# Optimization experiments

Hardware: AMD Instinct MI355X
Metric: run time of the kernel (lower is better)

## Reference

```python
import jax, jax.numpy as jnp
import numpy as np

N_NODES = 100000


def _gcn_norm(edge_index, num_nodes):
    # add self loops
    src, dst = edge_index[0], edge_index[1]
    loop = jnp.arange(num_nodes, dtype=src.dtype)
    row = jnp.concatenate([src, loop])  # [E+N]
    col = jnp.concatenate([dst, loop])
    ew = jnp.ones(row.shape[0], dtype=jnp.float32)
    deg = jax.ops.segment_sum(ew, col, num_segments=num_nodes)  # [N]
    dinv = jnp.where(deg > 0, jax.lax.rsqrt(deg), 0.0)
    norm = dinv[row] * ew * dinv[col]  # [E+N]
    return row, col, norm


def setup_inputs() -> dict:
    key = jax.random.key(0)
    k1, k2, k3 = jax.random.split(key, 3)
    x = jax.random.normal(k1, (N_NODES, 64), dtype=jnp.float32)
    edge_index = jax.random.randint(k2, (2, 1280000), 0, N_NODES, dtype=jnp.int64)
    W = jax.random.normal(k3, (40, 64), dtype=jnp.float32) * (1.0 / np.sqrt(64))
    b = jnp.zeros((40,), dtype=jnp.float32)
    return {"x": x, "edge_index": edge_index, "W": W, "b": b}


def reference(x, edge_index, W, b):
    K = 3
    row, col, norm = _gcn_norm(edge_index, N_NODES)
    h = x
    for _ in range(K):
        # gather from source nodes, scale by symmetric norm, scatter-add to dst
        msg = norm[:, None] * h[row]  # [E+N, F]
        h = jax.ops.segment_sum(msg, col, num_segments=N_NODES)
    logits = h @ W.T + b  # [N, C]
    return jax.nn.log_softmax(logits, axis=1)
```

## Files before the change

### kernel.cpp

```cpp
#include <hip/hip_runtime.h>

#define F_IN 64
#define F_OUT 40
#define USTRIDE 20
#define QPN 5

#define PART_BLK 256
#define PART_EPB 16
#define PART_TILE (PART_BLK * PART_EPB)
#define BSHIFT 8
#define BCAP 4096
#define MAXB 512

#define WSTRIDE 17

__device__ inline unsigned pk2(float x, float y) {
    unsigned a = __float_as_uint(x); a = (a + 0x7FFFu + ((a >> 16) & 1u)) >> 16;
    unsigned b = __float_as_uint(y); b = (b + 0x7FFFu + ((b >> 16) & 1u)) >> 16;
    return a | (b << 16);
}
__device__ inline void up2(unsigned u, float& a, float& b) {
    a = __uint_as_float(u << 16); b = __uint_as_float(u & 0xFFFF0000u);
}

__global__ void bucket_init_kernel(int* __restrict__ bfill, int nbk) {
    int b = blockIdx.x * blockDim.x + threadIdx.x;
    if (b < nbk) bfill[b] = b * BCAP;
}

__global__ __launch_bounds__(PART_BLK) void partition_kernel(const int* __restrict__ src,
                                                             const int* __restrict__ dst,
                                                             int* __restrict__ bfill,
                                                             unsigned* __restrict__ staging,
                                                             int E, int nbk) {
    __shared__ int hist[MAXB];
    __shared__ int base[MAXB];
    int tid = threadIdx.x;
    for (int b = tid; b < nbk; b += PART_BLK) hist[b] = 0;
    __syncthreads();

    int rank[PART_EPB];
    int bk[PART_EPB];
    unsigned rec[PART_EPB];
    int eb = blockIdx.x * PART_TILE + tid;
#pragma unroll
    for (int k = 0; k < PART_EPB; ++k) {
        int e = eb + k * PART_BLK;
        if (e < E) {
            int r = src[e];
            int c = dst[e];
            int b = c >> BSHIFT;
            bk[k] = b;
            rec[k] = (unsigned)r | ((unsigned)(c & 255) << 17);
            rank[k] = atomicAdd(&hist[b], 1);
        } else {
            bk[k] = -1;
        }
    }
    __syncthreads();
    for (int b = tid; b < nbk; b += PART_BLK) {
        int h = hist[b];
        base[b] = h ? atomicAdd(&bfill[b], h) : 0;
    }
    __syncthreads();
#pragma unroll
    for (int k = 0; k < PART_EPB; ++k) {
        if (bk[k] >= 0) staging[base[bk[k]] + rank[k]] = rec[k];
    }
}

__global__ __launch_bounds__(512) void btotal_scan_kernel(const int* __restrict__ bfill,
                                                          int* __restrict__ ebase,
                                                          int* __restrict__ rowptr_end,
                                                          int nbk, int E) {
    __shared__ int s[512];
    int tid = threadIdx.x;
    int v = (tid < nbk) ? (bfill[tid] - tid * BCAP) : 0;
    s[tid] = v;
    __syncthreads();
    for (int off = 1; off < 512; off <<= 1) {
        int t = (tid >= off) ? s[tid - off] : 0;
        __syncthreads();
        s[tid] += t;
        __syncthreads();
    }
    if (tid < nbk) ebase[tid] = s[tid] - v;
    if (tid == 0) *rowptr_end = E;
}

__global__ __launch_bounds__(256) void bucket_finalize_kernel(const unsigned* __restrict__ staging,
                                                              const int* __restrict__ bfill,
                                                              const int* __restrict__ ebase,
                                                              int* __restrict__ rowptr,
                                                              int* __restrict__ deg,
                                                              float* __restrict__ dinv,
                                                              float* __restrict__ dinv2,
                                                              int* __restrict__ srcs, int n) {
    int b = blockIdx.x;
    __shared__ int h[256];
    __shared__ int cur[256];
    int tid = threadIdx.x;
    h[tid] = 0;
    __syncthreads();

    int cnt = bfill[b] - b * BCAP;
    const unsigned* rec = staging + (size_t)b * BCAP;
    for (int i = tid; i < cnt; i += 256) {
        atomicAdd(&h[rec[i] >> 17], 1);
    }
    __syncthreads();

    int v = h[tid];
    for (int off = 1; off < 256; off <<= 1) {
        int t = (tid >= off) ? h[tid - off] : 0;
        __syncthreads();
        h[tid] += t;
        __syncthreads();
    }
    int excl = h[tid] - v;
    int base = ebase[b];
    int node = (b << BSHIFT) | tid;
    if (node < n) {
        rowptr[node] = base + excl;
        deg[node] = v;
        float r = rsqrtf((float)v + 1.0f);
        dinv[node] = r;
        dinv2[node] = r * r;
    }
    cur[tid] = base + excl;
    __syncthreads();

    for (int i = tid; i < cnt; i += 256) {
        unsigned rv = rec[i];
        int pos = atomicAdd(&cur[rv >> 17], 1);
        srcs[pos] = (int)(rv & 0x1FFFFu);
    }
}

__global__ __launch_bounds__(256, 6) void proj_kernel(const float* __restrict__ x,
                                                      const float* __restrict__ W,
                                                      const float* __restrict__ dinv,
                                                      unsigned* __restrict__ u, int n) {
    __shared__ float Ws[F_OUT * WSTRIDE * 4];
    for (int i = threadIdx.x; i < F_OUT * F_IN; i += 256) {
        int c = i >> 6;
        int k = i & 63;
        Ws[c * (WSTRIDE * 4) + k] = W[i];
    }
    __syncthreads();

    int t = blockIdx.x * 256 + threadIdx.x;
    int node = t >> 2;
    int q = t & 3;
    if (node >= n) return;

    const float4* xp = (const float4*)(x + (size_t)node * F_IN);
    const float4* Wq = (const float4*)Ws + (size_t)(q * 10) * WSTRIDE;

    float acc[10];
#pragma unroll
    for (int c = 0; c < 10; ++c) acc[c] = 0.0f;

#pragma unroll 1
    for (int f4 = 0; f4 < F_IN / 4; ++f4) {
        float4 xv = xp[f4];
#pragma unroll
        for (int c = 0; c < 10; ++c) {
            float4 w = Wq[c * WSTRIDE + f4];
            acc[c] += xv.x * w.x + xv.y * w.y + xv.z * w.z + xv.w * w.w;
        }
    }

    float dv = dinv[node];
    unsigned* up = u + (size_t)node * USTRIDE + q * 5;
#pragma unroll
    for (int j = 0; j < 5; ++j) {
        up[j] = pk2(dv * acc[2 * j], dv * acc[2 * j + 1]);
    }
}

__global__ __launch_bounds__(256) void propagate_kernel(const int* __restrict__ rowptr,
                                                        const int* __restrict__ srcs,
                                                        const float* __restrict__ dinv2,
                                                        const unsigned* __restrict__ ucur,
                                                        unsigned* __restrict__ unew, int n) {
    int t = blockIdx.x * blockDim.x + threadIdx.x;
    int node = t / QPN;
    int q = t - node * QPN;
    if (node >= n) return;

    int beg = rowptr[node];
    int end = rowptr[node + 1];

    const uint4* U = (const uint4*)ucur;
    uint4 sv = U[(size_t)node * QPN + q];
    float a0, a1, a2, a3, a4, a5, a6, a7;
    up2(sv.x, a0, a1); up2(sv.y, a2, a3); up2(sv.z, a4, a5); up2(sv.w, a6, a7);

    int i = beg;
    for (; i + 3 < end; i += 4) {
        int s0 = srcs[i], s1 = srcs[i + 1], s2 = srcs[i + 2], s3 = srcs[i + 3];
        uint4 v0 = U[(size_t)s0 * QPN + q];
        uint4 v1 = U[(size_t)s1 * QPN + q];
        uint4 v2 = U[(size_t)s2 * QPN + q];
        uint4 v3 = U[(size_t)s3 * QPN + q];
        float b0, b1;
        up2(v0.x, b0, b1); a0 += b0; a1 += b1;
        up2(v0.y, b0, b1); a2 += b0; a3 += b1;
        up2(v0.z, b0, b1); a4 += b0; a5 += b1;
        up2(v0.w, b0, b1); a6 += b0; a7 += b1;
        up2(v1.x, b0, b1); a0 += b0; a1 += b1;
        up2(v1.y, b0, b1); a2 += b0; a3 += b1;
        up2(v1.z, b0, b1); a4 += b0; a5 += b1;
        up2(v1.w, b0, b1); a6 += b0; a7 += b1;
        up2(v2.x, b0, b1); a0 += b0; a1 += b1;
        up2(v2.y, b0, b1); a2 += b0; a3 += b1;
        up2(v2.z, b0, b1); a4 += b0; a5 += b1;
        up2(v2.w, b0, b1); a6 += b0; a7 += b1;
        up2(v3.x, b0, b1); a0 += b0; a1 += b1;
        up2(v3.y, b0, b1); a2 += b0; a3 += b1;
        up2(v3.z, b0, b1); a4 += b0; a5 += b1;
        up2(v3.w, b0, b1); a6 += b0; a7 += b1;
    }
    for (; i < end; ++i) {
        uint4 v = U[(size_t)srcs[i] * QPN + q];
        float b0, b1;
        up2(v.x, b0, b1); a0 += b0; a1 += b1;
        up2(v.y, b0, b1); a2 += b0; a3 += b1;
        up2(v.z, b0, b1); a4 += b0; a5 += b1;
        up2(v.w, b0, b1); a6 += b0; a7 += b1;
    }

    float ds = dinv2[node];
    uint4 o;
    o.x = pk2(ds * a0, ds * a1);
    o.y = pk2(ds * a2, ds * a3);
    o.z = pk2(ds * a4, ds * a5);
    o.w = pk2(ds * a6, ds * a7);
    ((uint4*)unew)[(size_t)node * QPN + q] = o;
}

__global__ void logsoftmax_kernel(const unsigned* __restrict__ u, float* __restrict__ out,
                                  const float* __restrict__ bias,
                                  const int* __restrict__ deg, int n) {
    int node = blockIdx.x * blockDim.x + threadIdx.x;
    if (node >= n) return;
    float sq = sqrtf((float)deg[node] + 1.0f);
    const uint4* up = (const uint4*)(u + (size_t)node * USTRIDE);
    float v[F_OUT];
#pragma unroll
    for (int g = 0; g < 5; ++g) {
        uint4 t = up[g];
        float a, b2;
        up2(t.x, a, b2); v[8 * g + 0] = sq * a + bias[8 * g + 0];
                         v[8 * g + 1] = sq * b2 + bias[8 * g + 1];
        up2(t.y, a, b2); v[8 * g + 2] = sq * a + bias[8 * g + 2];
                         v[8 * g + 3] = sq * b2 + bias[8 * g + 3];
        up2(t.z, a, b2); v[8 * g + 4] = sq * a + bias[8 * g + 4];
                         v[8 * g + 5] = sq * b2 + bias[8 * g + 5];
        up2(t.w, a, b2); v[8 * g + 6] = sq * a + bias[8 * g + 6];
                         v[8 * g + 7] = sq * b2 + bias[8 * g + 7];
    }
    float mx = -1e30f;
#pragma unroll
    for (int c = 0; c < F_OUT; ++c) mx = fmaxf(mx, v[c]);
    float se = 0.0f;
#pragma unroll
    for (int c = 0; c < F_OUT; ++c) se += __expf(v[c] - mx);
    float lse = mx + __logf(se);
    float4* p = (float4*)(out + (size_t)node * F_OUT);
#pragma unroll
    for (int c4 = 0; c4 < F_OUT / 4; ++c4) {
        float4 t;
        t.x = v[4 * c4 + 0] - lse; t.y = v[4 * c4 + 1] - lse;
        t.z = v[4 * c4 + 2] - lse; t.w = v[4 * c4 + 3] - lse;
        p[c4] = t;
    }
}

extern "C" void kernel_launch(void* const* d_in, const int* in_sizes, int n_in,
                              void* d_out, int out_size, void* d_ws, size_t ws_size,
                              hipStream_t stream) {
    const float* x  = (const float*)d_in[0];
    const int*   ei = (const int*)d_in[1];
    const float* W  = (const float*)d_in[2];
    const float* b  = (const float*)d_in[3];

    const int N = in_sizes[0] / F_IN;
    const int E = in_sizes[1] / 2;
    const int* src = ei;
    const int* dst = ei + E;
    const int nbk = (N + (1 << BSHIFT) - 1) >> BSHIFT;

    char* base = (char*)d_ws;
    size_t off = 0;
    auto alloc = [&](size_t bytes) {
        char* p = base + off;
        off = (off + bytes + 255) & ~(size_t)255;
        return p;
    };
    int*      deg_i   = (int*)     alloc((size_t)N * 4);
    float*    dinv    = (float*)   alloc((size_t)N * 4);
    float*    dinv2   = (float*)   alloc((size_t)N * 4);
    int*      rowptr  = (int*)     alloc((size_t)(N + 1) * 4);
    int*      bfill   = (int*)     alloc((size_t)MAXB * 4);
    int*      ebase   = (int*)     alloc((size_t)MAXB * 4);
    unsigned* staging = (unsigned*)alloc((size_t)nbk * BCAP * 4);
    int*      srcs_s  = (int*)     alloc((size_t)E * 4);
    unsigned* uA      = (unsigned*)alloc((size_t)N * USTRIDE * 4);
    unsigned* uB      = (unsigned*)alloc((size_t)N * USTRIDE * 4);
    float*    outp    = (float*)d_out;

    bucket_init_kernel<<<(nbk + 255) / 256, 256, 0, stream>>>(bfill, nbk);
    partition_kernel<<<(E + PART_TILE - 1) / PART_TILE, PART_BLK, 0, stream>>>(
        src, dst, bfill, staging, E, nbk);

    btotal_scan_kernel<<<1, 512, 0, stream>>>(bfill, ebase, rowptr + N, nbk, E);
    bucket_finalize_kernel<<<nbk, 256, 0, stream>>>(staging, bfill, ebase, rowptr,
                                                    deg_i, dinv, dinv2, srcs_s, N);

    proj_kernel<<<((size_t)N * 4 + 255) / 256, 256, 0, stream>>>(x, W, dinv, uA, N);

    const int pt = N * QPN;
    const int pg = (pt + 255) / 256;
    propagate_kernel<<<pg, 256, 0, stream>>>(rowptr, srcs_s, dinv2, uA, uB, N);
    propagate_kernel<<<pg, 256, 0, stream>>>(rowptr, srcs_s, dinv2, uB, uA, N);
    propagate_kernel<<<pg, 256, 0, stream>>>(rowptr, srcs_s, dinv2, uA, uB, N);

    logsoftmax_kernel<<<(N + 255) / 256, 256, 0, stream>>>(uB, outp, b, deg_i, N);
}
```

Before: 218.1 us.

## Degree-sort nodes within buckets for propagation and process two nodes per thread in projection

Measured after the change: 245.1 us. 1.12x slower.

```diff
diff --git a/kernel.cpp b/kernel.cpp
--- a/kernel.cpp
+++ b/kernel.cpp
@@ -21,11 +21,6 @@
 }
 __device__ inline void up2(unsigned u, float& a, float& b) {
     a = __uint_as_float(u << 16); b = __uint_as_float(u & 0xFFFF0000u);
-}
-
-__global__ void bucket_init_kernel(int* __restrict__ bfill, int nbk) {
-    int b = blockIdx.x * blockDim.x + threadIdx.x;
-    if (b < nbk) bfill[b] = b * BCAP;
 }
 
 __global__ __launch_bounds__(PART_BLK) void partition_kernel(const int* __restrict__ src,
@@ -60,7 +55,7 @@
     __syncthreads();
     for (int b = tid; b < nbk; b += PART_BLK) {
         int h = hist[b];
-        base[b] = h ? atomicAdd(&bfill[b], h) : 0;
+        base[b] = h ? (b * BCAP + atomicAdd(&bfill[b], h)) : 0;
     }
     __syncthreads();
 #pragma unroll
@@ -75,7 +70,7 @@
                                                           int nbk, int E) {
     __shared__ int s[512];
     int tid = threadIdx.x;
-    int v = (tid < nbk) ? (bfill[tid] - tid * BCAP) : 0;
+    int v = (tid < nbk) ? bfill[tid] : 0;
     s[tid] = v;
     __syncthreads();
     for (int off = 1; off < 512; off <<= 1) {
@@ -95,15 +90,17 @@
                                                               int* __restrict__ deg,
                                                               float* __restrict__ dinv,
                                                               float* __restrict__ dinv2,
-                                                              int* __restrict__ srcs, int n) {
+                                                              int* __restrict__ srcs,
+                                                              int* __restrict__ perm, int n) {
     int b = blockIdx.x;
     __shared__ int h[256];
     __shared__ int cur[256];
+    __shared__ unsigned keys[256];
     int tid = threadIdx.x;
     h[tid] = 0;
     __syncthreads();
 
-    int cnt = bfill[b] - b * BCAP;
+    int cnt = bfill[b];
     const unsigned* rec = staging + (size_t)b * BCAP;
     for (int i = tid; i < cnt; i += 256) {
         atomicAdd(&h[rec[i] >> 17], 1);
@@ -111,6 +108,8 @@
     __syncthreads();
 
     int v = h[tid];
+    keys[tid] = ((unsigned)v << 8) | (unsigned)(255 - tid);
+
     for (int off = 1; off < 256; off <<= 1) {
         int t = (tid >= off) ? h[tid - off] : 0;
         __syncthreads();
@@ -135,9 +134,27 @@
         int pos = atomicAdd(&cur[rv >> 17], 1);
         srcs[pos] = (int)(rv & 0x1FFFFu);
     }
-}
-
-__global__ __launch_bounds__(256, 6) void proj_kernel(const float* __restrict__ x,
+    __syncthreads();
+
+    for (int k = 2; k <= 256; k <<= 1) {
+        for (int j = k >> 1; j > 0; j >>= 1) {
+            int p = tid ^ j;
+            if (p > tid) {
+                unsigned a = keys[tid];
+                unsigned c = keys[p];
+                bool asc_region = ((tid & k) == 0);
+                if (asc_region ? (a < c) : (a > c)) {
+                    keys[tid] = c;
+                    keys[p] = a;
+                }
+            }
+            __syncthreads();
+        }
+    }
+    perm[(b << BSHIFT) | tid] = (b << BSHIFT) | (int)(255u - (keys[tid] & 255u));
+}
+
+__global__ __launch_bounds__(256, 4) void proj_kernel(const float* __restrict__ x,
                                                       const float* __restrict__ W,
                                                       const float* __restrict__ dinv,
                                                       unsigned* __restrict__ u, int n) {
@@ -150,44 +167,54 @@
     __syncthreads();
 
     int t = blockIdx.x * 256 + threadIdx.x;
-    int node = t >> 2;
+    int g = t >> 2;
     int q = t & 3;
-    if (node >= n) return;
-
-    const float4* xp = (const float4*)(x + (size_t)node * F_IN);
-    const float4* Wq = (const float4*)Ws + (size_t)(q * 10) * WSTRIDE;
-
-    float acc[10];
-#pragma unroll
-    for (int c = 0; c < 10; ++c) acc[c] = 0.0f;
+    int n0 = 2 * g;
+    if (n0 >= n) return;
+    int n1 = n0 + 1;
+
+    const float4* xp0 = (const float4*)(x + (size_t)n0 * F_IN);
+    const float4* xp1 = (const float4*)(x + (size_t)n1 * F_IN);
+    const float4* Wq  = (const float4*)Ws + (size_t)(q * 10) * WSTRIDE;
+
+    float acc0[10], acc1[10];
+#pragma unroll
+    for (int c = 0; c < 10; ++c) { acc0[c] = 0.0f; acc1[c] = 0.0f; }
 
 #pragma unroll 1
     for (int f4 = 0; f4 < F_IN / 4; ++f4) {
-        float4 xv = xp[f4];
+        float4 x0 = xp0[f4];
+        float4 x1 = xp1[f4];
 #pragma unroll
         for (int c = 0; c < 10; ++c) {
             float4 w = Wq[c * WSTRIDE + f4];
-            acc[c] += xv.x * w.x + xv.y * w.y + xv.z * w.z + xv.w * w.w;
+            acc0[c] += x0.x * w.x + x0.y * w.y + x0.z * w.z + x0.w * w.w;
+            acc1[c] += x1.x * w.x + x1.y * w.y + x1.z * w.z + x1.w * w.w;
         }
     }
 
-    float dv = dinv[node];
-    unsigned* up = u + (size_t)node * USTRIDE + q * 5;
+    float d0 = dinv[n0];
+    float d1 = dinv[n1];
+    unsigned* up0 = u + (size_t)n0 * USTRIDE + q * 5;
+    unsigned* up1 = u + (size_t)n1 * USTRIDE + q * 5;
 #pragma unroll
     for (int j = 0; j < 5; ++j) {
-        up[j] = pk2(dv * acc[2 * j], dv * acc[2 * j + 1]);
-    }
-}
-
-__global__ __launch_bounds__(256) void propagate_kernel(const int* __restrict__ rowptr,
+        up0[j] = pk2(d0 * acc0[2 * j], d0 * acc0[2 * j + 1]);
+        up1[j] = pk2(d1 * acc1[2 * j], d1 * acc1[2 * j + 1]);
+    }
+}
+
+__global__ __launch_bounds__(256) void propagate_kernel(const int* __restrict__ perm,
+                                                        const int* __restrict__ rowptr,
                                                         const int* __restrict__ srcs,
                                                         const float* __restrict__ dinv2,
                                                         const unsigned* __restrict__ ucur,
                                                         unsigned* __restrict__ unew, int n) {
     int t = blockIdx.x * blockDim.x + threadIdx.x;
-    int node = t / QPN;
-    int q = t - node * QPN;
-    if (node >= n) return;
+    int g = t / QPN;
+    int q = t - g * QPN;
+    if (g >= n) return;
+    int node = perm[g];
 
     int beg = rowptr[node];
     int end = rowptr[node + 1];
@@ -305,27 +332,28 @@
     int*      rowptr  = (int*)     alloc((size_t)(N + 1) * 4);
     int*      bfill   = (int*)     alloc((size_t)MAXB * 4);
     int*      ebase   = (int*)     alloc((size_t)MAXB * 4);
+    int*      perm    = (int*)     alloc((size_t)(nbk << BSHIFT) * 4);
     unsigned* staging = (unsigned*)alloc((size_t)nbk * BCAP * 4);
     int*      srcs_s  = (int*)     alloc((size_t)E * 4);
     unsigned* uA      = (unsigned*)alloc((size_t)N * USTRIDE * 4);
     unsigned* uB      = (unsigned*)alloc((size_t)N * USTRIDE * 4);
     float*    outp    = (float*)d_out;
 
-    bucket_init_kernel<<<(nbk + 255) / 256, 256, 0, stream>>>(bfill, nbk);
+    hipMemsetAsync(bfill, 0, (size_t)nbk * 4, stream);
     partition_kernel<<<(E + PART_TILE - 1) / PART_TILE, PART_BLK, 0, stream>>>(
         src, dst, bfill, staging, E, nbk);
 
     btotal_scan_kernel<<<1, 512, 0, stream>>>(bfill, ebase, rowptr + N, nbk, E);
     bucket_finalize_kernel<<<nbk, 256, 0, stream>>>(staging, bfill, ebase, rowptr,
-                                                    deg_i, dinv, dinv2, srcs_s, N);
-
-    proj_kernel<<<((size_t)N * 4 + 255) / 256, 256, 0, stream>>>(x, W, dinv, uA, N);
+                                                    deg_i, dinv, dinv2, srcs_s, perm, N);
+
+    proj_kernel<<<((size_t)N * 2 + 255) / 256, 256, 0, stream>>>(x, W, dinv, uA, N);
 
     const int pt = N * QPN;
     const int pg = (pt + 255) / 256;
-    propagate_kernel<<<pg, 256, 0, stream>>>(rowptr, srcs_s, dinv2, uA, uB, N);
-    propagate_kernel<<<pg, 256, 0, stream>>>(rowptr, srcs_s, dinv2, uB, uA, N);
-    propagate_kernel<<<pg, 256, 0, stream>>>(rowptr, srcs_s, dinv2, uA, uB, N);
+    propagate_kernel<<<pg, 256, 0, stream>>>(perm, rowptr, srcs_s, dinv2, uA, uB, N);
+    propagate_kernel<<<pg, 256, 0, stream>>>(perm, rowptr, srcs_s, dinv2, uB, uA, N);
+    propagate_kernel<<<pg, 256, 0, stream>>>(perm, rowptr, srcs_s, dinv2, uA, uB, N);
 
     logsoftmax_kernel<<<(N + 255) / 256, 256, 0, stream>>>(uB, outp, b, deg_i, N);
 }
```
